# Optimization experiments

Hardware: AMD Instinct MI355X
Metric: run time of the kernel (lower is better)

The kernel has to match this reference:

```python
import jax, jax.numpy as jnp
import numpy as np

D_MODEL = 1024
H = 16
DK = D_MODEL // H
B, S = 2, 2048
NEG = -1e9


def setup_inputs() -> dict:
    key = jax.random.key(0)
    ks = jax.random.split(key, 7)
    scale = 1.0 / np.sqrt(D_MODEL)
    inp = {
        "q": jax.random.normal(ks[0], (B, S, D_MODEL), jnp.float32),
        "k": jax.random.normal(ks[1], (B, S, D_MODEL), jnp.float32),
        "v": jax.random.normal(ks[2], (B, S, D_MODEL), jnp.float32),
        # causal mask, broadcastable to (B, H, S, S); positions with 0 are masked
        "mask": jnp.tril(jnp.ones((S, S), dtype=bool))[None, None, :, :],
        "w_q": jax.random.normal(ks[3], (D_MODEL, D_MODEL), jnp.float32) * scale,
        "w_k": jax.random.normal(ks[4], (D_MODEL, D_MODEL), jnp.float32) * scale,
        "w_v": jax.random.normal(ks[5], (D_MODEL, D_MODEL), jnp.float32) * scale,
        "w_o": jax.random.normal(ks[6], (D_MODEL, D_MODEL), jnp.float32) * scale,
    }
    return inp


def reference(q, k, v, mask, w_q, w_k, w_v, w_o):
    # Linear projections (nn.Linear with bias=False: x @ W.T)
    query = q @ w_q.T  # (B, S, d_model)
    key_ = k @ w_k.T
    value = v @ w_v.T
    # split heads -> (B, h, S, dk)
    def split(x):
        return x.reshape(x.shape[0], x.shape[1], H, DK).transpose(0, 2, 1, 3)
    qh, kh, vh = split(query), split(key_), split(value)
    # scaled dot-product attention with full score materialization
    scores = jnp.einsum("bhqd,bhkd->bhqk", qh, kh) / jnp.sqrt(jnp.float32(DK))
    scores = jnp.where(mask, scores, NEG)
    attn = jax.nn.softmax(scores, axis=-1)  # (B, h, S, S); dropout p=0.0 -> identity
    out = jnp.einsum("bhqk,bhkd->bhqd", attn, vh)
    # merge heads -> (B, S, d_model)
    out = out.transpose(0, 2, 1, 3).reshape(out.shape[0], -1, H * DK)
    return out @ w_o.T
```

## Files before the change

### kernel.cpp

```cpp
#include <hip/hip_runtime.h>
#include <cstdint>
#include <cstddef>

typedef __bf16 bf16;
typedef __attribute__((ext_vector_type(4))) __bf16 bf16x4;
typedef __attribute__((ext_vector_type(8))) __bf16 bf16x8;
typedef __attribute__((ext_vector_type(4))) float floatx4;
typedef __attribute__((ext_vector_type(4))) short short4v;

#define MFMA16(a, b, c) __builtin_amdgcn_mfma_f32_16x16x32_bf16((a), (b), (c), 0, 0, 0)

__device__ __forceinline__ floatx4 MFMAK16(bf16x4 a, bf16x4 b, floatx4 c) {
#if __has_builtin(__builtin_amdgcn_mfma_f32_16x16x16bf16_1k)
  return __builtin_amdgcn_mfma_f32_16x16x16bf16_1k(
      __builtin_bit_cast(short4v, a), __builtin_bit_cast(short4v, b), c, 0, 0, 0);
#else
  floatx4 d;
  asm("v_mfma_f32_16x16x16_bf16 %0, %1, %2, %3"
      : "=v"(d)
      : "v"(a), "v"(b), "v"(c));
  return d;
#endif
}

constexpr int DMODEL = 1024;
constexpr int NH = 16;
constexpr int DKH = 64;
constexpr int B_ = 2;
constexpr int S_ = 2048;
constexpr int MTOT = B_ * S_;
constexpr float CEXP = 0.125f * 1.44269504f;

__device__ __forceinline__ void load_lds16(const void* g, void* l) {
  __builtin_amdgcn_global_load_lds(
      (const __attribute__((address_space(1))) uint32_t*)g,
      (__attribute__((address_space(3))) uint32_t*)l, 16, 0, 0);
}

__device__ __forceinline__ bf16x8 frag64(const bf16* lds, int row, int p) {
  int s = p ^ (row & 7);
  return *(const bf16x8*)&lds[row * 64 + s * 8];
}
__device__ __forceinline__ bf16x4 frag64h(const bf16* lds, int row, int p, int h) {
  int s = p ^ (row & 7);
  return *(const bf16x4*)&lds[row * 64 + s * 8 + h * 4];
}

__device__ __forceinline__ void stage32_bf16(const bf16* __restrict__ src,
                                             bf16* lds, int wave, int lane,
                                             int ldg) {
#pragma unroll
  for (int i = 0; i < 2; ++i) {
    int cb = (wave * 2 + i) * 64;
    int c = cb + lane;
    int r = c >> 2;
    int s = (c & 3) ^ ((r >> 1) & 3);
    load_lds16(&src[(size_t)r * ldg + s * 8], &lds[cb * 8]);
  }
}
__device__ __forceinline__ bf16x8 frag32_bf16(const bf16* lds, int row,
                                              int quad) {
  int s = quad ^ ((row >> 1) & 3);
  return *(const bf16x8*)&lds[row * 32 + s * 8];
}
__device__ __forceinline__ void stage32_f32(const float* __restrict__ src,
                                            float* lds, int wave, int lane,
                                            int ldg) {
#pragma unroll
  for (int i = 0; i < 4; ++i) {
    int cb = (wave * 4 + i) * 64;
    int c = cb + lane;
    int r = c >> 3;
    int s = (c & 7) ^ (r & 7);
    load_lds16(&src[(size_t)r * ldg + s * 4], &lds[cb * 4]);
  }
}
__device__ __forceinline__ bf16x8 frag32_f32(const float* lds, int row,
                                             int quad) {
  int s1 = (2 * quad) ^ (row & 7);
  int s2 = (2 * quad + 1) ^ (row & 7);
  float4 a = *(const float4*)&lds[row * 32 + s1 * 4];
  float4 b = *(const float4*)&lds[row * 32 + s2 * 4];
  bf16x8 h = {(bf16)a.x, (bf16)a.y, (bf16)a.z, (bf16)a.w,
              (bf16)b.x, (bf16)b.y, (bf16)b.z, (bf16)b.w};
  return h;
}

__global__ __launch_bounds__(256) void convert_kernel(
    const float* __restrict__ q, const float* __restrict__ k,
    const float* __restrict__ v, const float* __restrict__ wq,
    const float* __restrict__ wk, const float* __restrict__ wv,
    const float* __restrict__ wo, bf16* __restrict__ qb, bf16* __restrict__ kb,
    bf16* __restrict__ vb, bf16* __restrict__ wqb, bf16* __restrict__ wkb,
    bf16* __restrict__ wvb, bf16* __restrict__ wob) {
  const int bid = blockIdx.x;
  int seg, rel;
  if (bid < 6144) {
    seg = bid >> 11;
    rel = bid & 2047;
  } else {
    int t = bid - 6144;
    seg = 3 + (t >> 9);
    rel = t & 511;
  }
  const float* src;
  bf16* dst;
  switch (seg) {
    case 0: src = q;  dst = qb;  break;
    case 1: src = k;  dst = kb;  break;
    case 2: src = v;  dst = vb;  break;
    case 3: src = wq; dst = wqb; break;
    case 4: src = wk; dst = wkb; break;
    case 5: src = wv; dst = wvb; break;
    default: src = wo; dst = wob; break;
  }
  size_t idx = ((size_t)rel * 256 + threadIdx.x) * 8;
  float4 f0 = *(const float4*)&src[idx];
  float4 f1 = *(const float4*)&src[idx + 4];
  bf16x8 h = {(bf16)f0.x, (bf16)f0.y, (bf16)f0.z, (bf16)f0.w,
              (bf16)f1.x, (bf16)f1.y, (bf16)f1.z, (bf16)f1.w};
  *(bf16x8*)&dst[idx] = h;
}

template <typename TC>
__device__ __forceinline__ void gemm64(const bf16* __restrict__ A,
                                       const bf16* __restrict__ W,
                                       TC* __restrict__ C,
                                       bf16* __restrict__ vt, int K,
                                       int m0, int n0, float ascale) {
  constexpr int N = DMODEL;
  __shared__ alignas(16) bf16 smem[128 * 136];
  bf16* As = smem;
  bf16* Bs = smem + 128 * 64;

  const int tid = threadIdx.x;
  const int wave = tid >> 6;
  const int lane = tid & 63;
  const int quad = lane >> 4;
  const int l16 = lane & 15;
  const int wm = (wave >> 1) * 64;
  const int wn = (wave & 1) * 64;

  floatx4 acc[4][4] = {};

  for (int k0 = 0; k0 < K; k0 += 64) {
#pragma unroll
    for (int i = 0; i < 4; ++i) {
      int cb = (wave * 4 + i) * 64;
      int c = cb + lane;
      int r = c >> 3;
      int s = (c & 7) ^ (r & 7);
      load_lds16(&A[(size_t)(m0 + r) * K + k0 + s * 8], &As[cb * 8]);
      load_lds16(&W[(size_t)(n0 + r) * K + k0 + s * 8], &Bs[cb * 8]);
    }
    __syncthreads();

#pragma unroll
    for (int kk = 0; kk < 2; ++kk) {
      bf16x8 af[4], bfv[4];
#pragma unroll
      for (int mi = 0; mi < 4; ++mi)
        af[mi] = frag64(As, wm + mi * 16 + l16, kk * 4 + quad);
#pragma unroll
      for (int ni = 0; ni < 4; ++ni)
        bfv[ni] = frag64(Bs, wn + ni * 16 + l16, kk * 4 + quad);
#pragma unroll
      for (int mi = 0; mi < 4; ++mi)
#pragma unroll
        for (int ni = 0; ni < 4; ++ni)
          acc[mi][ni] = MFMA16(af[mi], bfv[ni], acc[mi][ni]);
    }
    __syncthreads();
  }

  if (vt) {
    bf16* T = smem;
#pragma unroll
    for (int mi = 0; mi < 4; ++mi)
#pragma unroll
      for (int ni = 0; ni < 4; ++ni) {
        int row = wm + mi * 16 + quad * 4;
        int col = wn + ni * 16 + l16;
        bf16x4 vvv = {(bf16)acc[mi][ni][0], (bf16)acc[mi][ni][1],
                      (bf16)acc[mi][ni][2], (bf16)acc[mi][ni][3]};
        *(bf16x4*)&T[col * 136 + row] = vvv;
      }
    __syncthreads();
    const int bb = m0 >> 11;
    const int sbase = (m0 & 2047) + l16 * 8;
#pragma unroll
    for (int jj = 0; jj < 8; ++jj) {
      int colv = wave * 32 + jj * 4 + quad;
      int gcol = n0 + colv;
      int h = gcol >> 6, d = gcol & 63;
      bf16x8 rowv = *(const bf16x8*)&T[colv * 136 + l16 * 8];
      *(bf16x8*)&vt[(size_t)((bb * NH + h) * DKH + d) * S_ + sbase] = rowv;
    }
  } else {
#pragma unroll
    for (int mi = 0; mi < 4; ++mi)
#pragma unroll
      for (int ni = 0; ni < 4; ++ni)
#pragma unroll
        for (int r = 0; r < 4; ++r) {
          int row = m0 + wm + mi * 16 + quad * 4 + r;
          int col = n0 + wn + ni * 16 + l16;
          C[(size_t)row * N + col] = (TC)(acc[mi][ni][r] * ascale);
        }
  }
}

__global__ __launch_bounds__(256, 3) void qkv64_kernel(
    const bf16* __restrict__ q, const bf16* __restrict__ k,
    const bf16* __restrict__ v, const bf16* __restrict__ wq,
    const bf16* __restrict__ wk, const bf16* __restrict__ wv,
    bf16* __restrict__ Q, bf16* __restrict__ K, bf16* __restrict__ Vt) {
  const int bid = blockIdx.x;
  const int xcd = bid & 7;
  const int j = bid >> 3;
  const int n = j & 7;
  const int rowslot = j >> 3;
  const int p = xcd * 12 + rowslot;
  const int z = p >> 5;
  const int y = p & 31;

  const bf16* A = (z == 0) ? q : (z == 1) ? k : v;
  const bf16* W = (z == 0) ? wq : (z == 1) ? wk : wv;
  bf16* C = (z == 0) ? Q : K;
  gemm64<bf16>(A, W, (z == 2) ? nullptr : C, (z == 2) ? Vt : nullptr,
               DMODEL, y * 128, n * 128, (z == 0) ? CEXP : 1.0f);
}

__global__ __launch_bounds__(256) void oproj64_kernel(
    const bf16* __restrict__ A, const bf16* __restrict__ W,
    float* __restrict__ C) {
  constexpr int K = DMODEL;
  constexpr int N = DMODEL;
  __shared__ alignas(16) bf16 As[64 * 64];
  __shared__ alignas(16) bf16 Bs[128 * 64];

  const int bid = blockIdx.x;
  const int xcd = bid & 7;
  const int j = bid >> 3;
  const int n = j & 7;
  const int slot = j >> 3;
  const int mt = xcd * 8 + slot;
  const int m0 = mt * 64;
  const int n0 = n * 128;

  const int tid = threadIdx.x;
  const int wave = tid >> 6;
  const int lane = tid & 63;
  const int quad = lane >> 4;
  const int l16 = lane & 15;
  const int wm = (wave >> 1) * 32;
  const int wn = (wave & 1) * 64;

  floatx4 acc[2][4] = {};

  for (int k0 = 0; k0 < K; k0 += 64) {
#pragma unroll
    for (int i = 0; i < 2; ++i) {
      int cb = (wave * 2 + i) * 64;
      int c = cb + lane;
      int r = c >> 3;
      int s = (c & 7) ^ (r & 7);
      load_lds16(&A[(size_t)(m0 + r) * K + k0 + s * 8], &As[cb * 8]);
    }
#pragma unroll
    for (int i = 0; i < 4; ++i) {
      int cb = (wave * 4 + i) * 64;
      int c = cb + lane;
      int r = c >> 3;
      int s = (c & 7) ^ (r & 7);
      load_lds16(&W[(size_t)(n0 + r) * K + k0 + s * 8], &Bs[cb * 8]);
    }
    __syncthreads();

#pragma unroll
    for (int kk = 0; kk < 2; ++kk) {
      bf16x8 af[2], bfv[4];
#pragma unroll
      for (int mi = 0; mi < 2; ++mi)
        af[mi] = frag64(As, wm + mi * 16 + l16, kk * 4 + quad);
#pragma unroll
      for (int ni = 0; ni < 4; ++ni)
        bfv[ni] = frag64(Bs, wn + ni * 16 + l16, kk * 4 + quad);
#pragma unroll
      for (int mi = 0; mi < 2; ++mi)
#pragma unroll
        for (int ni = 0; ni < 4; ++ni)
          acc[mi][ni] = MFMA16(af[mi], bfv[ni], acc[mi][ni]);
    }
    __syncthreads();
  }

#pragma unroll
  for (int mi = 0; mi < 2; ++mi)
#pragma unroll
    for (int ni = 0; ni < 4; ++ni)
#pragma unroll
      for (int r = 0; r < 4; ++r) {
        int row = m0 + wm + mi * 16 + quad * 4 + r;
        int col = n0 + wn + ni * 16 + l16;
        C[(size_t)row * N + col] = acc[mi][ni][r];
      }
}

template <typename TA, typename TW, typename TC>
__device__ __forceinline__ void gemm_core(const TA* __restrict__ A,
                                          const TW* __restrict__ W,
                                          TC* __restrict__ C,
                                          bf16* __restrict__ vt, int K,
                                          int m0, int n0, float ascale) {
  constexpr int N = DMODEL;
  __shared__ alignas(16) char smem[128 * 32 * (sizeof(TA) + sizeof(TW))];
  TA* As = (TA*)smem;
  TW* Bs = (TW*)(smem + 128 * 32 * sizeof(TA));

  const int tid = threadIdx.x;
  const int wave = tid >> 6;
  const int lane = tid & 63;
  const int quad = lane >> 4;
  const int l16 = lane & 15;
  const int wm = (wave >> 1) * 64;
  const int wn = (wave & 1) * 64;

  floatx4 acc[4][4] = {};

  for (int k0 = 0; k0 < K; k0 += 32) {
    if constexpr (sizeof(TA) == 2)
      stage32_bf16((const bf16*)A + (size_t)m0 * K + k0, (bf16*)As, wave, lane, K);
    else
      stage32_f32((const float*)A + (size_t)m0 * K + k0, (float*)As, wave, lane, K);
    if constexpr (sizeof(TW) == 2)
      stage32_bf16((const bf16*)W + (size_t)n0 * K + k0, (bf16*)Bs, wave, lane, K);
    else
      stage32_f32((const float*)W + (size_t)n0 * K + k0, (float*)Bs, wave, lane, K);
    __syncthreads();

    bf16x8 af[4], bfv[4];
#pragma unroll
    for (int mi = 0; mi < 4; ++mi) {
      if constexpr (sizeof(TA) == 2)
        af[mi] = frag32_bf16((const bf16*)As, wm + mi * 16 + l16, quad);
      else
        af[mi] = frag32_f32((const float*)As, wm + mi * 16 + l16, quad);
    }
#pragma unroll
    for (int ni = 0; ni < 4; ++ni) {
      if constexpr (sizeof(TW) == 2)
        bfv[ni] = frag32_bf16((const bf16*)Bs, wn + ni * 16 + l16, quad);
      else
        bfv[ni] = frag32_f32((const float*)Bs, wn + ni * 16 + l16, quad);
    }
#pragma unroll
    for (int mi = 0; mi < 4; ++mi)
#pragma unroll
      for (int ni = 0; ni < 4; ++ni)
        acc[mi][ni] = MFMA16(af[mi], bfv[ni], acc[mi][ni]);
    __syncthreads();
  }

  if (vt) {
#pragma unroll
    for (int mi = 0; mi < 4; ++mi)
#pragma unroll
      for (int ni = 0; ni < 4; ++ni)
#pragma unroll
        for (int r = 0; r < 4; ++r) {
          int row = m0 + wm + mi * 16 + quad * 4 + r;
          int col = n0 + wn + ni * 16 + l16;
          int bb = row >> 11, s = row & 2047;
          int h = col >> 6, d = col & 63;
          vt[(size_t)((bb * NH + h) * DKH + d) * S_ + s] = (bf16)acc[mi][ni][r];
        }
  } else {
#pragma unroll
    for (int mi = 0; mi < 4; ++mi)
#pragma unroll
      for (int ni = 0; ni < 4; ++ni)
#pragma unroll
        for (int r = 0; r < 4; ++r) {
          int row = m0 + wm + mi * 16 + quad * 4 + r;
          int col = n0 + wn + ni * 16 + l16;
          C[(size_t)row * N + col] = (TC)(acc[mi][ni][r] * ascale);
        }
  }
}

__global__ __launch_bounds__(256) void qkv_f32_kernel(
    const float* __restrict__ q, const float* __restrict__ k,
    const float* __restrict__ v, const float* __restrict__ wq,
    const float* __restrict__ wk, const float* __restrict__ wv,
    bf16* __restrict__ Q, bf16* __restrict__ K, bf16* __restrict__ Vt) {
  const int bid = blockIdx.x;
  const int xcd = bid & 7;
  const int j = bid >> 3;
  const int n = j & 7;
  const int rowslot = j >> 3;
  const int p = xcd * 12 + rowslot;
  const int z = p >> 5;
  const int y = p & 31;
  const float* A = (z == 0) ? q : (z == 1) ? k : v;
  const float* W = (z == 0) ? wq : (z == 1) ? wk : wv;
  bf16* C = (z == 0) ? Q : K;
  gemm_core<float, float, bf16>(A, W, (z == 2) ? nullptr : C,
                                (z == 2) ? Vt : nullptr, DMODEL, y * 128,
                                n * 128, (z == 0) ? CEXP : 1.0f);
}

__global__ __launch_bounds__(256) void oproj_f32_kernel(
    const bf16* __restrict__ A, const float* __restrict__ W,
    float* __restrict__ C) {
  const int bid = blockIdx.x;
  const int xcd = bid & 7;
  const int j = bid >> 3;
  const int n = j & 7;
  const int rowslot = j >> 3;
  const int y = xcd * 4 + rowslot;
  gemm_core<bf16, float, float>(A, W, C, nullptr, DMODEL, y * 128, n * 128,
                                1.0f);
}

__device__ __forceinline__ void stage_kv(const bf16* __restrict__ K,
                                         const bf16* __restrict__ Vt,
                                         bf16* Ks, bf16* Vts, size_t baseQ,
                                         size_t baseV, int kt, int wave,
                                         int lane) {
#pragma unroll
  for (int i = 0; i < 2; ++i) {
    int cb = (wave * 2 + i) * 64;
    int c = cb + lane;
    int r = c >> 3;
    int s = (c & 7) ^ (r & 7);
    load_lds16(&K[baseQ + (size_t)(kt * 64 + r) * DMODEL + s * 8], &Ks[cb * 8]);
    load_lds16(&Vt[baseV + (size_t)r * S_ + kt * 64 + s * 8], &Vts[cb * 8]);
  }
}

template <bool DIAG>
__device__ __forceinline__ void softmax4(const floatx4 sa[4], bf16x4 pb[4],
                                         float lp[4], int quad, int qb) {
#pragma unroll
  for (int kg = 0; kg < 4; ++kg) {
    float pv[4];
#pragma unroll
    for (int r = 0; r < 4; ++r) {
      float s = sa[kg][r];
      if (DIAG) {
        int key = kg * 16 + quad * 4 + r;
        s = (key > qb) ? -3.0e38f : s;
      }
      float p = __builtin_amdgcn_exp2f(s);
      lp[kg] += p;
      pv[r] = p;
    }
    pb[kg] = bf16x4{(bf16)pv[0], (bf16)pv[1], (bf16)pv[2], (bf16)pv[3]};
  }
}

template <bool DIAG>
__device__ __forceinline__ void attn_tile(const bf16* Ks, const bf16* Vts,
                                          const bf16x8 qf[2], floatx4 ot[4],
                                          float lp[4], int quad, int l16,
                                          int qb) {
  floatx4 sa[4] = {};
#pragma unroll
  for (int kk = 0; kk < 2; ++kk)
#pragma unroll
    for (int kg = 0; kg < 4; ++kg) {
      bf16x8 ka = frag64(Ks, kg * 16 + l16, kk * 4 + quad);
      sa[kg] = MFMA16(ka, qf[kk], sa[kg]);
    }
  bf16x4 pb[4];
  softmax4<DIAG>(sa, pb, lp, quad, qb);
#pragma unroll
  for (int kg = 0; kg < 4; ++kg)
#pragma unroll
    for (int di = 0; di < 4; ++di) {
      bf16x4 va = frag64h(Vts, di * 16 + l16, kg * 2 + (quad >> 1), quad & 1);
      ot[di] = MFMAK16(va, pb[kg], ot[di]);
    }
}

template <int LMODE>
__device__ __forceinline__ void pair_tile(const bf16* Ks, const bf16* Vts,
                                          const bf16x8 qfL[2],
                                          const bf16x8 qfH[2], floatx4 otL[4],
                                          floatx4 otH[4], float lpL[4],
                                          float lpH[4], int quad, int l16,
                                          int qb) {
  floatx4 saL[4] = {}, saH[4] = {};
#pragma unroll
  for (int kk = 0; kk < 2; ++kk)
#pragma unroll
    for (int kg = 0; kg < 4; ++kg) {
      bf16x8 ka = frag64(Ks, kg * 16 + l16, kk * 4 + quad);
      saL[kg] = MFMA16(ka, qfL[kk], saL[kg]);
      saH[kg] = MFMA16(ka, qfH[kk], saH[kg]);
    }
  bf16x4 pbL[4], pbH[4];
  if (LMODE == 1)
    softmax4<false>(saL, pbL, lpL, quad, qb);
  else
    softmax4<true>(saL, pbL, lpL, quad, qb);
  softmax4<false>(saH, pbH, lpH, quad, qb);
#pragma unroll
  for (int kg = 0; kg < 4; ++kg)
#pragma unroll
    for (int di = 0; di < 4; ++di) {
      bf16x4 va = frag64h(Vts, di * 16 + l16, kg * 2 + (quad >> 1), quad & 1);
      otL[di] = MFMAK16(va, pbL[kg], otL[di]);
      otH[di] = MFMAK16(va, pbH[kg], otH[di]);
    }
}

__global__ __launch_bounds__(256) void attn8_kernel(const bf16* __restrict__ Q,
                                                    const bf16* __restrict__ K,
                                                    const bf16* __restrict__ Vt,
                                                    bf16* __restrict__ O) {
  __shared__ alignas(16) bf16 Ks[2][64 * 64];
  __shared__ alignas(16) bf16 Vts[2][64 * 64];

  const int tid = threadIdx.x;
  const int wave = tid >> 6;
  const int lane = tid & 63;
  const int quad = lane >> 4;
  const int l16 = lane & 15;

  const int j = blockIdx.x;
  const int bh = j & 31;
  const int pr = j >> 5;
  const int qtL = pr;
  const int qtH = 31 - pr;
  const int h = bh & 15;
  const int b = bh >> 4;
  const size_t baseQ = (size_t)b * S_ * DMODEL + (size_t)h * DKH;
  const size_t baseV = (size_t)bh * DKH * S_;

  bf16x8 qfL[2], qfH[2];
#pragma unroll
  for (int kk = 0; kk < 2; ++kk) {
    qfL[kk] = *(const bf16x8*)&Q[baseQ +
        (size_t)(qtL * 64 + wave * 16 + l16) * DMODEL + kk * 32 + quad * 8];
    qfH[kk] = *(const bf16x8*)&Q[baseQ +
        (size_t)(qtH * 64 + wave * 16 + l16) * DMODEL + kk * 32 + quad * 8];
  }

  floatx4 otL[4] = {}, otH[4] = {};
  float lpL[4] = {}, lpH[4] = {};
  const int qb = wave * 16 + l16;

  stage_kv(K, Vt, Ks[0], Vts[0], baseQ, baseV, 0, wave, lane);
  __syncthreads();

  for (int kt = 0; kt < qtH; ++kt) {
    const int cur = kt & 1;
    stage_kv(K, Vt, Ks[cur ^ 1], Vts[cur ^ 1], baseQ, baseV, kt + 1, wave, lane);

    __builtin_amdgcn_s_setprio(1);
    if (kt < qtL)
      pair_tile<1>(Ks[cur], Vts[cur], qfL, qfH, otL, otH, lpL, lpH, quad, l16, qb);
    else if (kt == qtL)
      pair_tile<2>(Ks[cur], Vts[cur], qfL, qfH, otL, otH, lpL, lpH, quad, l16, qb);
    else
      attn_tile<false>(Ks[cur], Vts[cur], qfH, otH, lpH, quad, l16, qb);
    __builtin_amdgcn_s_setprio(0);

    __syncthreads();
  }
  {
    const int cur = qtH & 1;
    attn_tile<true>(Ks[cur], Vts[cur], qfH, otH, lpH, quad, l16, qb);
  }

  float lL = (lpL[0] + lpL[1]) + (lpL[2] + lpL[3]);
  lL += __shfl_xor(lL, 16, 64);
  lL += __shfl_xor(lL, 32, 64);
  float lH = (lpH[0] + lpH[1]) + (lpH[2] + lpH[3]);
  lH += __shfl_xor(lH, 16, 64);
  lH += __shfl_xor(lH, 32, 64);
  const float invL = 1.0f / lL;
  const float invH = 1.0f / lH;

  const size_t orowL = baseQ + (size_t)(qtL * 64 + wave * 16 + l16) * DMODEL;
  const size_t orowH = baseQ + (size_t)(qtH * 64 + wave * 16 + l16) * DMODEL;
#pragma unroll
  for (int di = 0; di < 4; ++di)
#pragma unroll
    for (int r = 0; r < 4; ++r) {
      O[orowL + di * 16 + quad * 4 + r] = (bf16)(otL[di][r] * invL);
      O[orowH + di * 16 + quad * 4 + r] = (bf16)(otH[di][r] * invH);
    }
}

extern "C" void kernel_launch(void* const* d_in, const int* in_sizes, int n_in,
                              void* d_out, int out_size, void* d_ws,
                              size_t ws_size, hipStream_t stream) {
  const float* q = (const float*)d_in[0];
  const float* k = (const float*)d_in[1];
  const float* v = (const float*)d_in[2];
  const float* wq = (const float*)d_in[4];
  const float* wk = (const float*)d_in[5];
  const float* wv = (const float*)d_in[6];
  const float* wo = (const float*)d_in[7];
  float* out = (float*)d_out;

  const size_t MB = 1024 * 1024;
  char* base = (char*)d_ws;
  bf16* Qp = (bf16*)(base);
  bf16* Kp = (bf16*)(base + 8 * MB);
  bf16* VtG = (bf16*)(base + 16 * MB);
  bf16* AO = (bf16*)(base + 24 * MB);

  if (ws_size >= 64 * MB) {
    bf16* qb = (bf16*)(base + 32 * MB);
    bf16* kb = (bf16*)(base + 40 * MB);
    bf16* vb = (bf16*)(base + 48 * MB);
    bf16* wqb = (bf16*)(base + 56 * MB);
    bf16* wkb = (bf16*)(base + 58 * MB);
    bf16* wvb = (bf16*)(base + 60 * MB);
    bf16* wob = (bf16*)(base + 62 * MB);
    convert_kernel<<<dim3(8192), 256, 0, stream>>>(
        q, k, v, wq, wk, wv, wo, qb, kb, vb, wqb, wkb, wvb, wob);
    qkv64_kernel<<<dim3(768), 256, 0, stream>>>(
        qb, kb, vb, wqb, wkb, wvb, Qp, Kp, VtG);
    attn8_kernel<<<dim3(512), 256, 0, stream>>>(Qp, Kp, VtG, AO);
    oproj64_kernel<<<dim3(512), 256, 0, stream>>>(AO, wob, out);
  } else {
    qkv_f32_kernel<<<dim3(768), 256, 0, stream>>>(
        q, k, v, wq, wk, wv, Qp, Kp, VtG);
    attn8_kernel<<<dim3(512), 256, 0, stream>>>(Qp, Kp, VtG, AO);
    oproj_f32_kernel<<<dim3(256), 256, 0, stream>>>(AO, wo, out);
  }
}
```

Before: 207.9 us.

## Process four query tiles per block with key-split waves and LDS reduction

The attention kernel now runs 512-thread blocks. Each block owns four causal query tiles: two short ones and two long ones for balance. The 8 waves split into 4 query-row slices times 2 key halves, so each staged K/V tile is reused across four query tiles, and K/V fragments are loaded once per iteration and shared. Partial outputs and row sums from the two key halves are combined through shared memory at the end. The aim is better K/V reuse and fewer blocks, at the cost of more registers (four accumulator sets), a 64KB shared buffer, and extra reduction syncs.

```diff
diff --git a/kernel.cpp b/kernel.cpp
--- a/kernel.cpp
+++ b/kernel.cpp
@@ -423,176 +423,173 @@
                                 1.0f);
 }
 
-__device__ __forceinline__ void stage_kv(const bf16* __restrict__ K,
-                                         const bf16* __restrict__ Vt,
-                                         bf16* Ks, bf16* Vts, size_t baseQ,
-                                         size_t baseV, int kt, int wave,
-                                         int lane) {
-#pragma unroll
-  for (int i = 0; i < 2; ++i) {
-    int cb = (wave * 2 + i) * 64;
-    int c = cb + lane;
-    int r = c >> 3;
-    int s = (c & 7) ^ (r & 7);
-    load_lds16(&K[baseQ + (size_t)(kt * 64 + r) * DMODEL + s * 8], &Ks[cb * 8]);
-    load_lds16(&Vt[baseV + (size_t)r * S_ + kt * 64 + s * 8], &Vts[cb * 8]);
-  }
+__device__ __forceinline__ void stage_one(const bf16* __restrict__ K,
+                                          const bf16* __restrict__ Vt,
+                                          bf16* Ks, bf16* Vts, size_t baseQ,
+                                          size_t baseV, int kt, int wave,
+                                          int lane) {
+  int cb = wave * 64;
+  int c = cb + lane;
+  int r = c >> 3;
+  int s = (c & 7) ^ (r & 7);
+  load_lds16(&K[baseQ + (size_t)(kt * 64 + r) * DMODEL + s * 8], &Ks[cb * 8]);
+  load_lds16(&Vt[baseV + (size_t)r * S_ + kt * 64 + s * 8], &Vts[cb * 8]);
 }
 
 template <bool DIAG>
-__device__ __forceinline__ void softmax4(const floatx4 sa[4], bf16x4 pb[4],
-                                         float lp[4], int quad, int qb) {
-#pragma unroll
-  for (int kg = 0; kg < 4; ++kg) {
+__device__ __forceinline__ void tile_half(const bf16x8 (&ka)[2][2],
+                                          const bf16x4 (&va)[2][4],
+                                          const bf16x8 qf[2], floatx4 (&ot)[4],
+                                          float& lp, int quad, int qb, int kh) {
+  floatx4 sa[2] = {};
+#pragma unroll
+  for (int kk = 0; kk < 2; ++kk)
+#pragma unroll
+    for (int kg = 0; kg < 2; ++kg)
+      sa[kg] = MFMA16(ka[kk][kg], qf[kk], sa[kg]);
+
+  bf16x4 pb[2];
+#pragma unroll
+  for (int kg = 0; kg < 2; ++kg) {
     float pv[4];
 #pragma unroll
     for (int r = 0; r < 4; ++r) {
       float s = sa[kg][r];
       if (DIAG) {
-        int key = kg * 16 + quad * 4 + r;
+        int key = kh * 32 + kg * 16 + quad * 4 + r;
         s = (key > qb) ? -3.0e38f : s;
       }
       float p = __builtin_amdgcn_exp2f(s);
-      lp[kg] += p;
+      lp += p;
       pv[r] = p;
     }
     pb[kg] = bf16x4{(bf16)pv[0], (bf16)pv[1], (bf16)pv[2], (bf16)pv[3]};
   }
-}
-
-template <bool DIAG>
-__device__ __forceinline__ void attn_tile(const bf16* Ks, const bf16* Vts,
-                                          const bf16x8 qf[2], floatx4 ot[4],
-                                          float lp[4], int quad, int l16,
-                                          int qb) {
-  floatx4 sa[4] = {};
-#pragma unroll
-  for (int kk = 0; kk < 2; ++kk)
-#pragma unroll
-    for (int kg = 0; kg < 4; ++kg) {
-      bf16x8 ka = frag64(Ks, kg * 16 + l16, kk * 4 + quad);
-      sa[kg] = MFMA16(ka, qf[kk], sa[kg]);
-    }
-  bf16x4 pb[4];
-  softmax4<DIAG>(sa, pb, lp, quad, qb);
-#pragma unroll
-  for (int kg = 0; kg < 4; ++kg)
-#pragma unroll
-    for (int di = 0; di < 4; ++di) {
-      bf16x4 va = frag64h(Vts, di * 16 + l16, kg * 2 + (quad >> 1), quad & 1);
-      ot[di] = MFMAK16(va, pb[kg], ot[di]);
-    }
-}
-
-template <int LMODE>
-__device__ __forceinline__ void pair_tile(const bf16* Ks, const bf16* Vts,
-                                          const bf16x8 qfL[2],
-                                          const bf16x8 qfH[2], floatx4 otL[4],
-                                          floatx4 otH[4], float lpL[4],
-                                          float lpH[4], int quad, int l16,
-                                          int qb) {
-  floatx4 saL[4] = {}, saH[4] = {};
-#pragma unroll
-  for (int kk = 0; kk < 2; ++kk)
-#pragma unroll
-    for (int kg = 0; kg < 4; ++kg) {
-      bf16x8 ka = frag64(Ks, kg * 16 + l16, kk * 4 + quad);
-      saL[kg] = MFMA16(ka, qfL[kk], saL[kg]);
-      saH[kg] = MFMA16(ka, qfH[kk], saH[kg]);
-    }
-  bf16x4 pbL[4], pbH[4];
-  if (LMODE == 1)
-    softmax4<false>(saL, pbL, lpL, quad, qb);
-  else
-    softmax4<true>(saL, pbL, lpL, quad, qb);
-  softmax4<false>(saH, pbH, lpH, quad, qb);
-#pragma unroll
-  for (int kg = 0; kg < 4; ++kg)
-#pragma unroll
-    for (int di = 0; di < 4; ++di) {
-      bf16x4 va = frag64h(Vts, di * 16 + l16, kg * 2 + (quad >> 1), quad & 1);
-      otL[di] = MFMAK16(va, pbL[kg], otL[di]);
-      otH[di] = MFMAK16(va, pbH[kg], otH[di]);
-    }
-}
-
-__global__ __launch_bounds__(256) void attn8_kernel(const bf16* __restrict__ Q,
-                                                    const bf16* __restrict__ K,
-                                                    const bf16* __restrict__ Vt,
-                                                    bf16* __restrict__ O) {
-  __shared__ alignas(16) bf16 Ks[2][64 * 64];
-  __shared__ alignas(16) bf16 Vts[2][64 * 64];
+
+#pragma unroll
+  for (int kg = 0; kg < 2; ++kg)
+#pragma unroll
+    for (int di = 0; di < 4; ++di)
+      ot[di] = MFMAK16(va[kg][di], pb[kg], ot[di]);
+}
+
+__global__ __launch_bounds__(512, 2) void attn12_kernel(
+    const bf16* __restrict__ Q, const bf16* __restrict__ K,
+    const bf16* __restrict__ Vt, bf16* __restrict__ O) {
+  __shared__ alignas(16) char smem[65536];
+  bf16* KsB = (bf16*)smem;
+  bf16* VtsB = (bf16*)(smem + 16384);
 
   const int tid = threadIdx.x;
   const int wave = tid >> 6;
   const int lane = tid & 63;
   const int quad = lane >> 4;
   const int l16 = lane & 15;
+  const int ws = wave >> 1;
+  const int kh = wave & 1;
 
   const int j = blockIdx.x;
   const int bh = j & 31;
-  const int pr = j >> 5;
-  const int qtL = pr;
-  const int qtH = 31 - pr;
+  const int pg = j >> 5;
+  const int qt[4] = {2 * pg, 2 * pg + 1, 30 - 2 * pg, 31 - 2 * pg};
   const int h = bh & 15;
   const int b = bh >> 4;
   const size_t baseQ = (size_t)b * S_ * DMODEL + (size_t)h * DKH;
   const size_t baseV = (size_t)bh * DKH * S_;
 
-  bf16x8 qfL[2], qfH[2];
-#pragma unroll
-  for (int kk = 0; kk < 2; ++kk) {
-    qfL[kk] = *(const bf16x8*)&Q[baseQ +
-        (size_t)(qtL * 64 + wave * 16 + l16) * DMODEL + kk * 32 + quad * 8];
-    qfH[kk] = *(const bf16x8*)&Q[baseQ +
-        (size_t)(qtH * 64 + wave * 16 + l16) * DMODEL + kk * 32 + quad * 8];
-  }
-
-  floatx4 otL[4] = {}, otH[4] = {};
-  float lpL[4] = {}, lpH[4] = {};
-  const int qb = wave * 16 + l16;
-
-  stage_kv(K, Vt, Ks[0], Vts[0], baseQ, baseV, 0, wave, lane);
+  bf16x8 qf[4][2];
+#pragma unroll
+  for (int t = 0; t < 4; ++t)
+#pragma unroll
+    for (int kk = 0; kk < 2; ++kk)
+      qf[t][kk] = *(const bf16x8*)&Q[baseQ +
+          (size_t)(qt[t] * 64 + ws * 16 + l16) * DMODEL + kk * 32 + quad * 8];
+
+  floatx4 ot[4][4] = {};
+  float lp[4] = {};
+  const int qb = ws * 16 + l16;
+
+  const int NIT = 32 - 2 * pg;
+
+  stage_one(K, Vt, KsB, VtsB, baseQ, baseV, 0, wave, lane);
   __syncthreads();
 
-  for (int kt = 0; kt < qtH; ++kt) {
+  for (int kt = 0; kt < NIT; ++kt) {
     const int cur = kt & 1;
-    stage_kv(K, Vt, Ks[cur ^ 1], Vts[cur ^ 1], baseQ, baseV, kt + 1, wave, lane);
+    if (kt + 1 < NIT)
+      stage_one(K, Vt, KsB + (cur ^ 1) * 4096, VtsB + (cur ^ 1) * 4096,
+                baseQ, baseV, kt + 1, wave, lane);
 
     __builtin_amdgcn_s_setprio(1);
-    if (kt < qtL)
-      pair_tile<1>(Ks[cur], Vts[cur], qfL, qfH, otL, otH, lpL, lpH, quad, l16, qb);
-    else if (kt == qtL)
-      pair_tile<2>(Ks[cur], Vts[cur], qfL, qfH, otL, otH, lpL, lpH, quad, l16, qb);
-    else
-      attn_tile<false>(Ks[cur], Vts[cur], qfH, otH, lpH, quad, l16, qb);
+    const bf16* ks = KsB + cur * 4096;
+    const bf16* vs = VtsB + cur * 4096;
+
+    bf16x8 ka[2][2];
+#pragma unroll
+    for (int kk = 0; kk < 2; ++kk)
+#pragma unroll
+      for (int kg = 0; kg < 2; ++kg)
+        ka[kk][kg] = frag64(ks, kh * 32 + kg * 16 + l16, kk * 4 + quad);
+    bf16x4 va[2][4];
+#pragma unroll
+    for (int kg = 0; kg < 2; ++kg)
+#pragma unroll
+      for (int di = 0; di < 4; ++di)
+        va[kg][di] = frag64h(vs, di * 16 + l16,
+                             (kh * 2 + kg) * 2 + (quad >> 1), quad & 1);
+
+#pragma unroll
+    for (int t = 0; t < 4; ++t) {
+      if (kt < qt[t])
+        tile_half<false>(ka, va, qf[t], ot[t], lp[t], quad, qb, kh);
+      else if (kt == qt[t])
+        tile_half<true>(ka, va, qf[t], ot[t], lp[t], quad, qb, kh);
+    }
     __builtin_amdgcn_s_setprio(0);
 
     __syncthreads();
   }
-  {
-    const int cur = qtH & 1;
-    attn_tile<true>(Ks[cur], Vts[cur], qfH, otH, lpH, quad, l16, qb);
-  }
-
-  float lL = (lpL[0] + lpL[1]) + (lpL[2] + lpL[3]);
-  lL += __shfl_xor(lL, 16, 64);
-  lL += __shfl_xor(lL, 32, 64);
-  float lH = (lpH[0] + lpH[1]) + (lpH[2] + lpH[3]);
-  lH += __shfl_xor(lH, 16, 64);
-  lH += __shfl_xor(lH, 32, 64);
-  const float invL = 1.0f / lL;
-  const float invH = 1.0f / lH;
-
-  const size_t orowL = baseQ + (size_t)(qtL * 64 + wave * 16 + l16) * DMODEL;
-  const size_t orowH = baseQ + (size_t)(qtH * 64 + wave * 16 + l16) * DMODEL;
-#pragma unroll
-  for (int di = 0; di < 4; ++di)
-#pragma unroll
-    for (int r = 0; r < 4; ++r) {
-      O[orowL + di * 16 + quad * 4 + r] = (bf16)(otL[di][r] * invL);
-      O[orowH + di * 16 + quad * 4 + r] = (bf16)(otH[di][r] * invH);
-    }
+
+  floatx4* ox = (floatx4*)smem;
+  if (kh == 1) {
+#pragma unroll
+    for (int t = 0; t < 4; ++t)
+#pragma unroll
+      for (int di = 0; di < 4; ++di)
+        ox[((ws * 4 + t) * 4 + di) * 64 + lane] = ot[t][di];
+  }
+  __syncthreads();
+  if (kh == 0) {
+#pragma unroll
+    for (int t = 0; t < 4; ++t)
+#pragma unroll
+      for (int di = 0; di < 4; ++di)
+        ot[t][di] += ox[((ws * 4 + t) * 4 + di) * 64 + lane];
+  }
+  __syncthreads();
+  float* lx = (float*)smem;
+  if (kh == 1) {
+#pragma unroll
+    for (int t = 0; t < 4; ++t)
+      lx[(ws * 4 + t) * 64 + lane] = lp[t];
+  }
+  __syncthreads();
+  if (kh == 0) {
+#pragma unroll
+    for (int t = 0; t < 4; ++t) {
+      float l = lp[t] + lx[(ws * 4 + t) * 64 + lane];
+      l += __shfl_xor(l, 16, 64);
+      l += __shfl_xor(l, 32, 64);
+      const float inv = 1.0f / l;
+      const size_t orow = baseQ +
+          (size_t)(qt[t] * 64 + ws * 16 + l16) * DMODEL;
+#pragma unroll
+      for (int di = 0; di < 4; ++di)
+#pragma unroll
+        for (int r = 0; r < 4; ++r)
+          O[orow + di * 16 + quad * 4 + r] = (bf16)(ot[t][di][r] * inv);
+    }
+  }
 }
 
 extern "C" void kernel_launch(void* const* d_in, const int* in_sizes, int n_in,
@@ -626,12 +623,12 @@
         q, k, v, wq, wk, wv, wo, qb, kb, vb, wqb, wkb, wvb, wob);
     qkv64_kernel<<<dim3(768), 256, 0, stream>>>(
         qb, kb, vb, wqb, wkb, wvb, Qp, Kp, VtG);
-    attn8_kernel<<<dim3(512), 256, 0, stream>>>(Qp, Kp, VtG, AO);
+    attn12_kernel<<<dim3(256), 512, 0, stream>>>(Qp, Kp, VtG, AO);
     oproj64_kernel<<<dim3(512), 256, 0, stream>>>(AO, wob, out);
   } else {
     qkv_f32_kernel<<<dim3(768), 256, 0, stream>>>(
         q, k, v, wq, wk, wv, Qp, Kp, VtG);
-    attn8_kernel<<<dim3(512), 256, 0, stream>>>(Qp, Kp, VtG, AO);
+    attn12_kernel<<<dim3(256), 512, 0, stream>>>(Qp, Kp, VtG, AO);
     oproj_f32_kernel<<<dim3(256), 256, 0, stream>>>(AO, wo, out);
   }
 }
```

After: 201.8 us. -2.9%, faster.

## Replace LDS-staged attention blocks with single-wave blocks loading K/V fragments directly

Applied to the files above, without the earlier changes.

The attention kernel moves from 256-thread blocks that double-buffer K and V tiles in shared memory to 64-thread single-wave blocks that load MFMA fragments straight from global memory into registers, double-buffered in two register sets. This removes LDS staging and the block-wide barriers. The grid is remapped so that blocks sharing a batch-head land on the same XCD and short and long query-tile pairs are interleaved, which is meant to improve L2 reuse and load balance. In exchange, each wave issues its own redundant global loads of K/V (four waves now read the same tile separately), register pressure rises, and there is no cross-wave sharing through LDS.

```diff
diff --git a/kernel.cpp b/kernel.cpp
--- a/kernel.cpp
+++ b/kernel.cpp
@@ -423,20 +423,27 @@
                                 1.0f);
 }
 
-__device__ __forceinline__ void stage_kv(const bf16* __restrict__ K,
-                                         const bf16* __restrict__ Vt,
-                                         bf16* Ks, bf16* Vts, size_t baseQ,
-                                         size_t baseV, int kt, int wave,
-                                         int lane) {
-#pragma unroll
-  for (int i = 0; i < 2; ++i) {
-    int cb = (wave * 2 + i) * 64;
-    int c = cb + lane;
-    int r = c >> 3;
-    int s = (c & 7) ^ (r & 7);
-    load_lds16(&K[baseQ + (size_t)(kt * 64 + r) * DMODEL + s * 8], &Ks[cb * 8]);
-    load_lds16(&Vt[baseV + (size_t)r * S_ + kt * 64 + s * 8], &Vts[cb * 8]);
-  }
+struct FragsT {
+  bf16x8 ka[2][4];
+  bf16x4 va[4][4];
+};
+
+__device__ __forceinline__ void load_frags(FragsT& f, const bf16* __restrict__ K,
+                                           const bf16* __restrict__ Vt,
+                                           size_t baseQ, size_t baseV, int kt,
+                                           int quad, int l16) {
+#pragma unroll
+  for (int kk = 0; kk < 2; ++kk)
+#pragma unroll
+    for (int kg = 0; kg < 4; ++kg)
+      f.ka[kk][kg] = *(const bf16x8*)&K[baseQ +
+          (size_t)(kt * 64 + kg * 16 + l16) * DMODEL + kk * 32 + quad * 8];
+#pragma unroll
+  for (int kg = 0; kg < 4; ++kg)
+#pragma unroll
+    for (int di = 0; di < 4; ++di)
+      f.va[kg][di] = *(const bf16x4*)&Vt[baseV +
+          (size_t)(di * 16 + l16) * S_ + kt * 64 + kg * 16 + quad * 4];
 }
 
 template <bool DIAG>
@@ -460,78 +467,49 @@
   }
 }
 
-template <bool DIAG>
-__device__ __forceinline__ void attn_tile(const bf16* Ks, const bf16* Vts,
-                                          const bf16x8 qf[2], floatx4 ot[4],
-                                          float lp[4], int quad, int l16,
-                                          int qb) {
-  floatx4 sa[4] = {};
-#pragma unroll
-  for (int kk = 0; kk < 2; ++kk)
-#pragma unroll
-    for (int kg = 0; kg < 4; ++kg) {
-      bf16x8 ka = frag64(Ks, kg * 16 + l16, kk * 4 + quad);
-      sa[kg] = MFMA16(ka, qf[kk], sa[kg]);
-    }
-  bf16x4 pb[4];
-  softmax4<DIAG>(sa, pb, lp, quad, qb);
-#pragma unroll
-  for (int kg = 0; kg < 4; ++kg)
-#pragma unroll
-    for (int di = 0; di < 4; ++di) {
-      bf16x4 va = frag64h(Vts, di * 16 + l16, kg * 2 + (quad >> 1), quad & 1);
-      ot[di] = MFMAK16(va, pb[kg], ot[di]);
-    }
-}
-
-template <int LMODE>
-__device__ __forceinline__ void pair_tile(const bf16* Ks, const bf16* Vts,
-                                          const bf16x8 qfL[2],
+template <int MODE>
+__device__ __forceinline__ void comp_unit(const FragsT& f, const bf16x8 qfL[2],
                                           const bf16x8 qfH[2], floatx4 otL[4],
                                           floatx4 otH[4], float lpL[4],
-                                          float lpH[4], int quad, int l16,
-                                          int qb) {
+                                          float lpH[4], int quad, int qb) {
   floatx4 saL[4] = {}, saH[4] = {};
 #pragma unroll
   for (int kk = 0; kk < 2; ++kk)
 #pragma unroll
     for (int kg = 0; kg < 4; ++kg) {
-      bf16x8 ka = frag64(Ks, kg * 16 + l16, kk * 4 + quad);
-      saL[kg] = MFMA16(ka, qfL[kk], saL[kg]);
-      saH[kg] = MFMA16(ka, qfH[kk], saH[kg]);
+      if (MODE <= 1) saL[kg] = MFMA16(f.ka[kk][kg], qfL[kk], saL[kg]);
+      saH[kg] = MFMA16(f.ka[kk][kg], qfH[kk], saH[kg]);
     }
   bf16x4 pbL[4], pbH[4];
-  if (LMODE == 1)
-    softmax4<false>(saL, pbL, lpL, quad, qb);
-  else
-    softmax4<true>(saL, pbL, lpL, quad, qb);
-  softmax4<false>(saH, pbH, lpH, quad, qb);
+  if (MODE == 0) softmax4<false>(saL, pbL, lpL, quad, qb);
+  if (MODE == 1) softmax4<true>(saL, pbL, lpL, quad, qb);
+  softmax4<MODE == 3>(saH, pbH, lpH, quad, qb);
 #pragma unroll
   for (int kg = 0; kg < 4; ++kg)
 #pragma unroll
     for (int di = 0; di < 4; ++di) {
-      bf16x4 va = frag64h(Vts, di * 16 + l16, kg * 2 + (quad >> 1), quad & 1);
-      otL[di] = MFMAK16(va, pbL[kg], otL[di]);
-      otH[di] = MFMAK16(va, pbH[kg], otH[di]);
-    }
-}
-
-__global__ __launch_bounds__(256) void attn8_kernel(const bf16* __restrict__ Q,
-                                                    const bf16* __restrict__ K,
-                                                    const bf16* __restrict__ Vt,
-                                                    bf16* __restrict__ O) {
-  __shared__ alignas(16) bf16 Ks[2][64 * 64];
-  __shared__ alignas(16) bf16 Vts[2][64 * 64];
-
-  const int tid = threadIdx.x;
-  const int wave = tid >> 6;
-  const int lane = tid & 63;
+      if (MODE <= 1) otL[di] = MFMAK16(f.va[kg][di], pbL[kg], otL[di]);
+      otH[di] = MFMAK16(f.va[kg][di], pbH[kg], otH[di]);
+    }
+}
+
+__global__ __launch_bounds__(64, 2) void attn13_kernel(
+    const bf16* __restrict__ Q, const bf16* __restrict__ K,
+    const bf16* __restrict__ Vt, bf16* __restrict__ O) {
+  const int lane = threadIdx.x;
   const int quad = lane >> 4;
   const int l16 = lane & 15;
 
-  const int j = blockIdx.x;
-  const int bh = j & 31;
-  const int pr = j >> 5;
+  const int bid = blockIdx.x;
+  const int xcd = bid & 7;
+  const int rest = bid >> 3;
+  const int ws = rest & 3;
+  const int sel = (rest >> 2) & 1;
+  const int pg = (rest >> 3) & 7;
+  const int bhh = rest >> 6;
+  const int bh = (bhh << 3) | xcd;
+  const int pr = sel ? (15 - pg) : pg;
+
   const int qtL = pr;
   const int qtH = 31 - pr;
   const int h = bh & 15;
@@ -543,37 +521,43 @@
 #pragma unroll
   for (int kk = 0; kk < 2; ++kk) {
     qfL[kk] = *(const bf16x8*)&Q[baseQ +
-        (size_t)(qtL * 64 + wave * 16 + l16) * DMODEL + kk * 32 + quad * 8];
+        (size_t)(qtL * 64 + ws * 16 + l16) * DMODEL + kk * 32 + quad * 8];
     qfH[kk] = *(const bf16x8*)&Q[baseQ +
-        (size_t)(qtH * 64 + wave * 16 + l16) * DMODEL + kk * 32 + quad * 8];
+        (size_t)(qtH * 64 + ws * 16 + l16) * DMODEL + kk * 32 + quad * 8];
   }
 
   floatx4 otL[4] = {}, otH[4] = {};
   float lpL[4] = {}, lpH[4] = {};
-  const int qb = wave * 16 + l16;
-
-  stage_kv(K, Vt, Ks[0], Vts[0], baseQ, baseV, 0, wave, lane);
-  __syncthreads();
-
-  for (int kt = 0; kt < qtH; ++kt) {
-    const int cur = kt & 1;
-    stage_kv(K, Vt, Ks[cur ^ 1], Vts[cur ^ 1], baseQ, baseV, kt + 1, wave, lane);
-
-    __builtin_amdgcn_s_setprio(1);
-    if (kt < qtL)
-      pair_tile<1>(Ks[cur], Vts[cur], qfL, qfH, otL, otH, lpL, lpH, quad, l16, qb);
-    else if (kt == qtL)
-      pair_tile<2>(Ks[cur], Vts[cur], qfL, qfH, otL, otH, lpL, lpH, quad, l16, qb);
-    else
-      attn_tile<false>(Ks[cur], Vts[cur], qfH, otH, lpH, quad, l16, qb);
-    __builtin_amdgcn_s_setprio(0);
-
-    __syncthreads();
-  }
-  {
-    const int cur = qtH & 1;
-    attn_tile<true>(Ks[cur], Vts[cur], qfH, otH, lpH, quad, l16, qb);
-  }
+  const int qb = ws * 16 + l16;
+
+#define COMP_UNIT(f, kt)                                                     \
+  do {                                                                       \
+    __builtin_amdgcn_s_setprio(1);                                           \
+    if ((kt) < qtL)                                                          \
+      comp_unit<0>(f, qfL, qfH, otL, otH, lpL, lpH, quad, qb);               \
+    else if ((kt) == qtL)                                                    \
+      comp_unit<1>(f, qfL, qfH, otL, otH, lpL, lpH, quad, qb);               \
+    else if ((kt) < qtH)                                                     \
+      comp_unit<2>(f, qfL, qfH, otL, otH, lpL, lpH, quad, qb);               \
+    else                                                                     \
+      comp_unit<3>(f, qfL, qfH, otL, otH, lpL, lpH, quad, qb);               \
+    __builtin_amdgcn_s_setprio(0);                                           \
+  } while (0)
+
+  FragsT fA, fB;
+  load_frags(fA, K, Vt, baseQ, baseV, 0, quad, l16);
+  int kt = 0;
+  for (;;) {
+    if (kt + 1 <= qtH) load_frags(fB, K, Vt, baseQ, baseV, kt + 1, quad, l16);
+    COMP_UNIT(fA, kt);
+    ++kt;
+    if (kt > qtH) break;
+    if (kt + 1 <= qtH) load_frags(fA, K, Vt, baseQ, baseV, kt + 1, quad, l16);
+    COMP_UNIT(fB, kt);
+    ++kt;
+    if (kt > qtH) break;
+  }
+#undef COMP_UNIT
 
   float lL = (lpL[0] + lpL[1]) + (lpL[2] + lpL[3]);
   lL += __shfl_xor(lL, 16, 64);
@@ -584,8 +568,8 @@
   const float invL = 1.0f / lL;
   const float invH = 1.0f / lH;
 
-  const size_t orowL = baseQ + (size_t)(qtL * 64 + wave * 16 + l16) * DMODEL;
-  const size_t orowH = baseQ + (size_t)(qtH * 64 + wave * 16 + l16) * DMODEL;
+  const size_t orowL = baseQ + (size_t)(qtL * 64 + ws * 16 + l16) * DMODEL;
+  const size_t orowH = baseQ + (size_t)(qtH * 64 + ws * 16 + l16) * DMODEL;
 #pragma unroll
   for (int di = 0; di < 4; ++di)
 #pragma unroll
@@ -626,12 +610,12 @@
         q, k, v, wq, wk, wv, wo, qb, kb, vb, wqb, wkb, wvb, wob);
     qkv64_kernel<<<dim3(768), 256, 0, stream>>>(
         qb, kb, vb, wqb, wkb, wvb, Qp, Kp, VtG);
-    attn8_kernel<<<dim3(512), 256, 0, stream>>>(Qp, Kp, VtG, AO);
+    attn13_kernel<<<dim3(2048), 64, 0, stream>>>(Qp, Kp, VtG, AO);
     oproj64_kernel<<<dim3(512), 256, 0, stream>>>(AO, wob, out);
   } else {
     qkv_f32_kernel<<<dim3(768), 256, 0, stream>>>(
         q, k, v, wq, wk, wv, Qp, Kp, VtG);
-    attn8_kernel<<<dim3(512), 256, 0, stream>>>(Qp, Kp, VtG, AO);
+    attn13_kernel<<<dim3(2048), 64, 0, stream>>>(Qp, Kp, VtG, AO);
     oproj_f32_kernel<<<dim3(256), 256, 0, stream>>>(AO, wo, out);
   }
 }
```

New measurement: 322.9 us. 1.55x slower.
